# Optimization experiments

Measured on AMD Instinct MI355X. Metric: run time of the kernel, lower is better.

Reference implementation:

```python
import jax, jax.numpy as jnp
import numpy as np

NV, NA, T, FD, C, E = 192, 64, 128, 1024, 128, 262144
SPK = 3
N = (NV + NA) * T  # 32768 total graph nodes
NEG = -1e30


def _seg_max(msg, dst, mask):
    # masked scatter-max; PyG fills segments with no messages with 0
    m = jnp.where(mask[:, None], msg, NEG)
    out = jax.ops.segment_max(m, dst, num_segments=N)
    return jnp.where(out > NEG * 0.5, out, 0.0)


def _edge_conv(x, src, dst, mask, W1, b1, W2, b2):
    # EdgeConv: max_j MLP(cat[x_i, x_j - x_i])
    xi = x[dst]
    h = jnp.concatenate([xi, x[src] - xi], axis=-1)  # [E, 2C]
    h = jax.nn.relu(h @ W1 + b1) @ W2 + b2
    return _seg_max(h, dst, mask)


def _sage_conv(x, src, dst, mask, Wl, bl, Wr):
    # SAGEConv: lin_l(mean_j x_j) + lin_r(x_i), lin_r has no bias
    mf = mask.astype(x.dtype)
    s = jax.ops.segment_sum(x[src] * mf[:, None], dst, num_segments=N)
    cnt = jax.ops.segment_sum(mf, dst, num_segments=N)
    mean = s / jnp.maximum(cnt, 1.0)[:, None]
    return mean @ Wl + bl + x @ Wr


def setup_inputs():
    ks = jax.random.split(jax.random.key(0), 24)
    s = 0.05
    vals = jnp.array([-3, -2, -1, 0, 1, 3], jnp.int32)
    return {
        "x_visual": jax.random.normal(ks[0], (NV, T, FD), jnp.float32),
        "x_audio": jax.random.normal(ks[1], (NA, T, FD), jnp.float32),
        "W011": jax.random.normal(ks[2], (FD, C)) * s, "b011": jnp.zeros((C,)),
        "W012": jax.random.normal(ks[3], (FD, C)) * s, "b012": jnp.zeros((C,)),
        "ecA_W1": jax.random.normal(ks[4], (2 * C, C)) * s, "ecA_b1": jnp.zeros((C,)),
        "ecA_W2": jax.random.normal(ks[5], (C, C)) * s, "ecA_b2": jnp.zeros((C,)),
        "ec1_W1": jax.random.normal(ks[6], (2 * C, C)) * s, "ec1_b1": jnp.zeros((C,)),
        "ec1_W2": jax.random.normal(ks[7], (C, C)) * s, "ec1_b2": jnp.zeros((C,)),
        "ec2_W1": jax.random.normal(ks[8], (2 * C, C)) * s, "ec2_b1": jnp.zeros((C,)),
        "ec2_W2": jax.random.normal(ks[9], (C, C)) * s, "ec2_b2": jnp.zeros((C,)),
        "ec3_W1": jax.random.normal(ks[10], (2 * C, C)) * s, "ec3_b1": jnp.zeros((C,)),
        "ec3_W2": jax.random.normal(ks[11], (C, C)) * s, "ec3_b2": jnp.zeros((C,)),
        "sage_Wl": jax.random.normal(ks[12], (C, C)) * s, "sage_bl": jnp.zeros((C,)),
        "sage_Wr": jax.random.normal(ks[13], (C, C)) * s,
        "fc_W": jax.random.normal(ks[14], (C, 1)) * s, "fc_b": jnp.zeros((1,)),
        "edge_index": jax.random.randint(ks[15], (2, E), 0, N, dtype=jnp.int32),
        "edge_attr": vals[jax.random.randint(ks[16], (E,), 0, 6)],
        "speakers": SPK,
    }


def reference(x_visual, x_audio, W011, b011, W012, b012,
              ecA_W1, ecA_b1, ecA_W2, ecA_b2,
              ec1_W1, ec1_b1, ec1_W2, ec1_b2,
              ec2_W1, ec2_b1, ec2_W2, ec2_b2,
              ec3_W1, ec3_b1, ec3_W2, ec3_b2,
              sage_Wl, sage_bl, sage_Wr, fc_W, fc_b,
              edge_index, edge_attr, speakers):
    xv = x_visual @ W011 + b011          # [NV, T, C]
    xa = x_audio @ W012 + b012           # [NA, T, C]
    x = jnp.concatenate([xv, xa], axis=0).reshape(-1, C)  # [N, C]
    src, dst = edge_index[0], edge_index[1]
    m_audio = edge_attr == -2
    m_vpa = edge_attr == -3
    m_acv = edge_attr == 3
    m1 = (edge_attr >= 0) & (edge_attr <= 1)
    m2 = (edge_attr <= 0) & (edge_attr >= -1)
    m3 = jnp.abs(edge_attr) <= 1
    # Visual_Add_Audio_GNN: max-aggregate (x_i + x_j)
    xa_g = jax.nn.relu(_seg_max(x[dst] + x[src], dst, m_vpa))
    a = jax.nn.relu(_edge_conv(xa_g, src, dst, m_audio, ecA_W1, ecA_b1, ecA_W2, ecA_b2))
    a_res = a @ fc_W + fc_b              # [N, 1] per-node audio scores
    # Audio_Weight_Add_Visual_GNN: sum-aggregate (w_j * x_j + x_i)
    wmsg = jnp.where(m_acv[:, None], a_res[src] * x[src] + x[dst], 0.0)
    xv2 = jax.nn.relu(jax.ops.segment_sum(wmsg, dst, num_segments=N))

    def branch(mask, W1, b1, W2, b2):
        h = jax.nn.relu(_edge_conv(xv2, src, dst, mask, W1, b1, W2, b2))
        return jax.nn.relu(_sage_conv(h, src, dst, mask, sage_Wl, sage_bl, sage_Wr))

    xo = (branch(m1, ec1_W1, ec1_b1, ec1_W2, ec1_b2)
          + branch(m2, ec2_W1, ec2_b1, ec2_W2, ec2_b2)
          + branch(m3, ec3_W1, ec3_b1, ec3_W2, ec3_b2))
    # gather main-speaker visual nodes
    idx = (jnp.arange(0, NV * T, speakers * T)[:, None] + jnp.arange(T)).reshape(-1)
    return xo[idx]
```

## Files before the change

### kernel.cpp

```cpp
#include <hip/hip_runtime.h>
#include <cstdint>
#include <cstddef>

#define NVv 192
#define NAa 64
#define TT 128
#define FDd 1024
#define CCc 128
#define EEe 262144
#define NNn 32768

typedef _Float16 f16x8 __attribute__((ext_vector_type(8)));
typedef float f32x4 __attribute__((ext_vector_type(4)));

#define CAP0 65536
#define CAP1 65536
#define CAP2 65536
#define CAP3 98304
#define CAP4 98304
#define CAP5 147456
#define ARENA_TOTAL (CAP0+CAP1+CAP2+CAP3+CAP4+CAP5)
#define OFF0 0
#define OFF1 CAP0
#define OFF2 (CAP0+CAP1)
#define OFF3 (CAP0+CAP1+CAP2)
#define OFF4 (CAP0+CAP1+CAP2+CAP3)
#define OFF5 (CAP0+CAP1+CAP2+CAP3+CAP4)

__device__ __forceinline__ void eval_masks(int a, bool m[6]) {
    m[0] = (a == -3); m[1] = (a == -2); m[2] = (a == 3);
    m[3] = (a >= 0) & (a <= 1);
    m[4] = (a >= -1) & (a <= 0);
    m[5] = (a >= -1) & (a <= 1);
}

struct WSmall { const float* p[14]; };
struct PV3  { const _Float16* Wd[3]; const _Float16* Wv[3]; const float* b1[3];
              _Float16* P[3]; _Float16* V[3]; };
struct MLP3 { const _Float16* W2[3]; const float* b2[3];
              const _Float16* P[3]; const _Float16* V[3]; float* AH[3]; };

__global__ __launch_bounds__(256) void k_setup(
    const float* __restrict__ W011, const float* __restrict__ W012,
    WSmall wsm, _Float16* __restrict__ WT, _Float16* __restrict__ WTs,
    float* __restrict__ hf)
{
    int blk = blockIdx.x, tid = threadIdx.x;
    if (blk < 1024) {
        int idx = blk * 256 + tid;
        int which = idx >> 17;
        int r = idx & 131071;
        int n = r >> 10, k = r & 1023;
        const float* src = which ? W012 : W011;
        WT[idx] = (_Float16)src[k * 128 + n];
    } else if (blk < 1920) {
        int idx = (blk - 1024) * 256 + tid;
        int seg = idx >> 14;
        int r = idx & 16383;
        int n = r >> 7, k = r & 127;
        const float* src = wsm.p[seg];
        float v = src[k * 128 + n];
        if (seg < 12 && (seg % 3) == 0) v -= src[16384 + k * 128 + n];
        WTs[idx] = (_Float16)v;
    } else {
        size_t i = (size_t)(blk - 1920) * 1024 + (size_t)tid * 4;
        *(float4*)(hf + i) = make_float4(0.f, 0.f, 0.f, 0.f);
    }
}

__global__ __launch_bounds__(256) void k_hist(
    const int* __restrict__ attr, const int* __restrict__ edst,
    int* __restrict__ hist)
{
    int e = blockIdx.x * 256 + threadIdx.x;
    int a = attr[e], d = edst[e];
    bool m[6]; eval_masks(a, m);
#pragma unroll
    for (int j = 0; j < 6; ++j)
        if (m[j]) atomicAdd(&hist[j * NNn + d], 1);
}

__global__ __launch_bounds__(256) void k_scan_a(
    const int* __restrict__ hist, int* __restrict__ base, int* __restrict__ bsum)
{
    __shared__ int wsum[4];
    int idx = blockIdx.x * 256 + threadIdx.x;
    int tid = threadIdx.x, lane = tid & 63, wv = tid >> 6;
    int v = hist[idx];
    int x = v;
#pragma unroll
    for (int off = 1; off < 64; off <<= 1) {
        int y = __shfl_up(x, off, 64);
        if (lane >= off) x += y;
    }
    if (lane == 63) wsum[wv] = x;
    __syncthreads();
    int add = 0;
    for (int w = 0; w < wv; ++w) add += wsum[w];
    base[idx] = add + x - v;
    if (tid == 255) bsum[blockIdx.x] = add + x;
}

__global__ __launch_bounds__(384) void k_scan_b(int* __restrict__ bsum, int* __restrict__ cnts)
{
    int wv = threadIdx.x >> 6;
    int lane = threadIdx.x & 63;
    int run = 0;
#pragma unroll
    for (int c0 = 0; c0 < 128; c0 += 64) {
        int v = bsum[wv * 128 + c0 + lane];
        int x = v;
#pragma unroll
        for (int off = 1; off < 64; off <<= 1) {
            int y = __shfl_up(x, off, 64);
            if (lane >= off) x += y;
        }
        bsum[wv * 128 + c0 + lane] = run + (x - v);
        run += __shfl(x, 63, 64);
    }
    if (lane == 0) cnts[wv] = run;
}

__global__ __launch_bounds__(256) void k_scan_c(int* __restrict__ base, const int* __restrict__ bsum)
{
    base[blockIdx.x * 256 + threadIdx.x] += bsum[blockIdx.x];
}

__global__ __launch_bounds__(256) void k_fill_zero(
    const int* __restrict__ esrc, const int* __restrict__ edst,
    const int* __restrict__ attr, const int* __restrict__ base,
    int* __restrict__ fill, int2* __restrict__ arena, const int* __restrict__ hist,
    float* __restrict__ AH0, float* __restrict__ AH1,
    float* __restrict__ AH2, float* __restrict__ AH3)
{
    int blk = blockIdx.x, tid = threadIdx.x;
    if (blk < 1024) {
        int e = blk * 256 + tid;
        int a = attr[e];
        int s = esrc[e], d = edst[e];
        bool m[6]; eval_masks(a, m);
        const int caps[6] = {CAP0, CAP1, CAP2, CAP3, CAP4, CAP5};
        const int offs[6] = {OFF0, OFF1, OFF2, OFF3, OFF4, OFF5};
#pragma unroll
        for (int j = 0; j < 6; ++j) {
            if (m[j]) {
                int pos = base[j * NNn + d] + atomicAdd(&fill[j * NNn + d], 1);
                if (pos < caps[j]) arena[offs[j] + pos] = make_int2(s, d);
            }
        }
    } else {
        int zb = blk - 1024;
        int col = tid & 127, sub = tid >> 7;
        const int js[4] = {1, 3, 4, 5};
        float* AHs[4] = {AH0, AH1, AH2, AH3};
        for (int d = zb * 2 + sub; d < NNn; d += 2048 * 2) {
#pragma unroll
            for (int jj = 0; jj < 4; ++jj) {
                int j = js[jj];
                int c = hist[j * NNn + d];
                bool need;
                if (c == 0) need = true;
                else {
                    int b = base[j * NNn + d], e = b + c;
                    need = ((b & 63) == 0) || ((e & 63) == 0) || ((b >> 6) != ((e - 1) >> 6));
                }
                if (need) AHs[jj][(size_t)d * 128 + col] = 0.f;
            }
        }
    }
}

__global__ __launch_bounds__(512) void k_proj(
    const float* __restrict__ xv, const float* __restrict__ xa,
    const _Float16* __restrict__ BTv, const _Float16* __restrict__ BTa,
    float* __restrict__ Pp0, float* __restrict__ Pp1)
{
    __shared__ _Float16 Bl[2][128][136];
    const int tid = threadIdx.x, wave = tid >> 6, lane = tid & 63;
    const int tile = blockIdx.x >> 1, kh = blockIdx.x & 1;
    const float* A; const _Float16* BT; int mbase, obase;
    if (tile < 192) { A = xv; BT = BTv; mbase = tile * 128; obase = mbase; }
    else { A = xa; BT = BTa; mbase = (tile - 192) * 128; obase = 24576 + mbase; }
    float* Pout = kh ? Pp1 : Pp0;
    const int kbase = kh * 512;

    const int mrow = mbase + wave * 16 + (lane & 15);
    const int fk   = (lane >> 4) * 8;
    f32x4 acc[8];
#pragma unroll
    for (int i = 0; i < 8; ++i) acc[i] = (f32x4){0,0,0,0};

#pragma unroll
    for (int it = 0; it < 4; ++it) {
        int c = it * 512 + tid;
        int n = c >> 4, koff = (c & 15) * 8;
        *(f16x8*)&Bl[0][n][koff] = *(const f16x8*)(BT + (size_t)n * 1024 + kbase + koff);
    }
    f16x8 af[4];
#pragma unroll
    for (int t4 = 0; t4 < 4; ++t4) {
        const float* asrc = A + (size_t)mrow * 1024 + kbase + t4 * 32 + fk;
        float4 a0 = *(const float4*)asrc;
        float4 a1 = *(const float4*)(asrc + 4);
        af[t4] = (f16x8){ (_Float16)a0.x, (_Float16)a0.y, (_Float16)a0.z, (_Float16)a0.w,
                          (_Float16)a1.x, (_Float16)a1.y, (_Float16)a1.z, (_Float16)a1.w };
    }
    __syncthreads();

    for (int kc = 0; kc < 4; ++kc) {
        const int cur = kc & 1;
        f16x8 nf[4];
        if (kc < 3) {
            const int nxt = cur ^ 1;
#pragma unroll
            for (int it = 0; it < 4; ++it) {
                int c = it * 512 + tid;
                int n = c >> 4, koff = (c & 15) * 8;
                *(f16x8*)&Bl[nxt][n][koff] =
                    *(const f16x8*)(BT + (size_t)n * 1024 + kbase + (kc + 1) * 128 + koff);
            }
#pragma unroll
            for (int t4 = 0; t4 < 4; ++t4) {
                const float* asrc = A + (size_t)mrow * 1024 + kbase + (kc + 1) * 128 + t4 * 32 + fk;
                float4 a0 = *(const float4*)asrc;
                float4 a1 = *(const float4*)(asrc + 4);
                nf[t4] = (f16x8){ (_Float16)a0.x, (_Float16)a0.y, (_Float16)a0.z, (_Float16)a0.w,
                                  (_Float16)a1.x, (_Float16)a1.y, (_Float16)a1.z, (_Float16)a1.w };
            }
        }
#pragma unroll
        for (int t4 = 0; t4 < 4; ++t4)
#pragma unroll
            for (int nt = 0; nt < 8; ++nt) {
                f16x8 bf = *(const f16x8*)&Bl[cur][nt * 16 + (lane & 15)][t4 * 32 + fk];
                acc[nt] = __builtin_amdgcn_mfma_f32_16x16x32_f16(af[t4], bf, acc[nt], 0, 0, 0);
            }
        if (kc < 3) {
#pragma unroll
            for (int t4 = 0; t4 < 4; ++t4) af[t4] = nf[t4];
        }
        __syncthreads();
    }
    const int cbase = lane & 15, rloc = (lane >> 4) * 4;
    const int wgrp = wave & 3;
    float* Hsf = (float*)&Bl[0][0][0] + (size_t)wgrp * 16 * 132;
#pragma unroll
    for (int grp = 0; grp < 2; ++grp) {
        if ((wave >> 2) == grp) {
#pragma unroll
            for (int nt = 0; nt < 8; ++nt) {
                int c2 = nt * 16 + cbase;
#pragma unroll
                for (int rr = 0; rr < 4; ++rr)
                    Hsf[(rloc + rr) * 132 + c2] = acc[nt][rr];
            }
#pragma unroll
            for (int it = 0; it < 8; ++it) {
                int id = it * 64 + lane;
                int row = id >> 5, off = (id & 31) * 4;
                float4 v = *(float4*)&Hsf[row * 132 + off];
                *(float4*)&Pout[(size_t)(obase + wave * 16 + row) * 128 + off] = v;
            }
        }
        __syncthreads();
    }
}

__global__ __launch_bounds__(256) void k_reduce(
    const float* __restrict__ Pp0, const float* __restrict__ Pp1,
    const float* __restrict__ b011, const float* __restrict__ b012,
    float* __restrict__ X)
{
    size_t f = (size_t)blockIdx.x * 256 + threadIdx.x;
    size_t i = f * 4;
    int col = (int)(i & 127);
    int row = (int)(i >> 7);
    const float* bias = (row < 24576) ? b011 : b012;
    float4 a = *(const float4*)(Pp0 + i);
    float4 b = *(const float4*)(Pp1 + i);
    float4 bb = *(const float4*)(bias + col);
    *(float4*)(X + i) = make_float4(a.x + b.x + bb.x, a.y + b.y + bb.y,
                                    a.z + b.z + bb.z, a.w + b.w + bb.w);
}

__device__ __forceinline__ void pv_body(
    const float* __restrict__ A, const _Float16* __restrict__ BT1,
    const float* __restrict__ b1, const _Float16* __restrict__ BT2,
    _Float16* __restrict__ P, _Float16* __restrict__ V, int tileblk,
    _Float16 (*Bl1)[136], _Float16 (*Bl2)[136], float* bb)
{
    const int tid = threadIdx.x, wave = tid >> 6, lane = tid & 63;
    const int r0 = tileblk * 64 + wave * 16;
    const int fk = (lane >> 4) * 8;
    const int mrow = r0 + (lane & 15);
    float4 a0[4], a1[4];
#pragma unroll
    for (int t4 = 0; t4 < 4; ++t4) {
        const float* asrc = A + (size_t)mrow * 128 + t4 * 32 + fk;
        a0[t4] = *(const float4*)asrc;
        a1[t4] = *(const float4*)(asrc + 4);
    }
#pragma unroll
    for (int it = 0; it < 8; ++it) {
        int c = it * 256 + tid;
        int n = c >> 4, koff = (c & 15) * 8;
        *(f16x8*)&Bl1[n][koff] = *(const f16x8*)(BT1 + (size_t)n * 128 + koff);
        *(f16x8*)&Bl2[n][koff] = *(const f16x8*)(BT2 + (size_t)n * 128 + koff);
    }
    if (tid < 128) bb[tid] = b1[tid];
    __syncthreads();

    f16x8 af[4];
#pragma unroll
    for (int t4 = 0; t4 < 4; ++t4)
        af[t4] = (f16x8){ (_Float16)a0[t4].x, (_Float16)a0[t4].y, (_Float16)a0[t4].z, (_Float16)a0[t4].w,
                          (_Float16)a1[t4].x, (_Float16)a1[t4].y, (_Float16)a1[t4].z, (_Float16)a1[t4].w };
    f32x4 acc1[8], acc2[8];
#pragma unroll
    for (int i = 0; i < 8; ++i) { acc1[i] = (f32x4){0,0,0,0}; acc2[i] = (f32x4){0,0,0,0}; }
#pragma unroll
    for (int t4 = 0; t4 < 4; ++t4)
#pragma unroll
        for (int nt = 0; nt < 8; ++nt) {
            f16x8 bf1 = *(const f16x8*)&Bl1[nt * 16 + (lane & 15)][t4 * 32 + fk];
            f16x8 bf2 = *(const f16x8*)&Bl2[nt * 16 + (lane & 15)][t4 * 32 + fk];
            acc1[nt] = __builtin_amdgcn_mfma_f32_16x16x32_f16(af[t4], bf1, acc1[nt], 0, 0, 0);
            acc2[nt] = __builtin_amdgcn_mfma_f32_16x16x32_f16(af[t4], bf2, acc2[nt], 0, 0, 0);
        }
    __syncthreads();
    _Float16* Hs = &Bl1[0][0] + (size_t)wave * 16 * 136;
    const int cbase = lane & 15, rloc = (lane >> 4) * 4;
#pragma unroll
    for (int nt = 0; nt < 8; ++nt) {
        int c2 = nt * 16 + cbase;
        float bvv = bb[c2];
#pragma unroll
        for (int rr = 0; rr < 4; ++rr)
            Hs[(rloc + rr) * 136 + c2] = (_Float16)(acc1[nt][rr] + bvv);
    }
#pragma unroll
    for (int it = 0; it < 4; ++it) {
        int id = it * 64 + lane;
        int row = id >> 4, koff = (id & 15) * 8;
        *(f16x8*)&P[(size_t)(r0 + row) * 128 + koff] = *(f16x8*)&Hs[row * 136 + koff];
    }
#pragma unroll
    for (int nt = 0; nt < 8; ++nt) {
        int c2 = nt * 16 + cbase;
#pragma unroll
        for (int rr = 0; rr < 4; ++rr)
            Hs[(rloc + rr) * 136 + c2] = (_Float16)acc2[nt][rr];
    }
#pragma unroll
    for (int it = 0; it < 4; ++it) {
        int id = it * 64 + lane;
        int row = id >> 4, koff = (id & 15) * 8;
        *(f16x8*)&V[(size_t)(r0 + row) * 128 + koff] = *(f16x8*)&Hs[row * 136 + koff];
    }
}

__global__ __launch_bounds__(256) void k_pv(
    const float* __restrict__ A, const _Float16* __restrict__ BT1,
    const float* __restrict__ b1, const _Float16* __restrict__ BT2,
    _Float16* __restrict__ P, _Float16* __restrict__ V)
{
    __shared__ _Float16 Bl1[128][136];
    __shared__ _Float16 Bl2[128][136];
    __shared__ float bb[128];
    pv_body(A, BT1, b1, BT2, P, V, blockIdx.x, Bl1, Bl2, bb);
}

__global__ __launch_bounds__(256) void k_pv3(const float* __restrict__ A, PV3 p)
{
    __shared__ _Float16 Bl1[128][136];
    __shared__ _Float16 Bl2[128][136];
    __shared__ float bb[128];
    int b = blockIdx.x >> 9, t = blockIdx.x & 511;
    pv_body(A, p.Wd[b], p.b1[b], p.Wv[b], p.P[b], p.V[b], t, Bl1, Bl2, bb);
}

__device__ __forceinline__ void mlp_tile(
    const _Float16* __restrict__ P, const _Float16* __restrict__ V,
    const _Float16* __restrict__ W2T, const float* __restrict__ b2,
    const int2* __restrict__ list, int cnt, int t, float* __restrict__ agg,
    _Float16 (*Rl)[136], _Float16 (*W2l)[136], float* b2l,
    int2* eSD, unsigned char* gstart, int* gdst, int* ngrS)
{
    const int tid  = threadIdx.x;
    const int wave = tid >> 6;
    const int lane = tid & 63;
#pragma unroll
    for (int i = 0; i < 8; ++i) {
        int c = tid + i * 256;
        int n = c >> 4, koff = (c & 15) * 8;
        *(f16x8*)&W2l[n][koff] = *(const f16x8*)(W2T + n * 128 + koff);
    }
    if (tid < 128) b2l[tid] = b2[tid];
    if (tid < 64) {
        int e = t * 64 + tid;
        eSD[tid] = (e < cnt) ? list[e] : make_int2(0, -1);
    }
    __syncthreads();
    if (tid < 64) {
        int d = eSD[tid].y;
        bool flag = (tid == 0) || (d != eSD[tid - 1].y);
        unsigned long long bm = __ballot(flag);
        int rank = (int)__popcll(bm & ((1ull << tid) - 1ull));
        if (flag) { gstart[rank] = (unsigned char)tid; gdst[rank] = d; }
        if (tid == 0) {
            int ng = (int)__popcll(bm);
            *ngrS = ng;
            gstart[ng] = 64;
        }
    }
    const int rrow = tid >> 4;
    const int rch  = (tid & 15) * 8;
#pragma unroll
    for (int p = 0; p < 4; ++p) {
        int i = p * 16 + rrow;
        int2 sd = eSD[i];
        f16x8 rv = {0, 0, 0, 0, 0, 0, 0, 0};
        if (sd.y >= 0) {
            f16x8 pv = *(const f16x8*)(P + (size_t)sd.y * 128 + rch);
            f16x8 vv = *(const f16x8*)(V + (size_t)sd.x * 128 + rch);
            rv = pv + vv;
#pragma unroll
            for (int q = 0; q < 8; ++q)
                rv[q] = (rv[q] > (_Float16)0.f) ? rv[q] : (_Float16)0.f;
        }
        *(f16x8*)&Rl[i][rch] = rv;
    }
    __syncthreads();

    const int frow  = wave * 16 + (lane & 15);
    const int fq    = (lane >> 4) * 8;
    f32x4 acc[8];
#pragma unroll
    for (int i = 0; i < 8; ++i) acc[i] = (f32x4){0,0,0,0};
#pragma unroll
    for (int t4 = 0; t4 < 4; ++t4) {
        f16x8 af = *(const f16x8*)&Rl[frow][t4 * 32 + fq];
#pragma unroll
        for (int nt = 0; nt < 8; ++nt) {
            f16x8 bf = *(const f16x8*)&W2l[nt * 16 + (lane & 15)][t4 * 32 + fq];
            acc[nt] = __builtin_amdgcn_mfma_f32_16x16x32_f16(af, bf, acc[nt], 0, 0, 0);
        }
    }
    __syncthreads();
    const int rbase = wave * 16 + (lane >> 4) * 4;
    const int cbase = lane & 15;
#pragma unroll
    for (int nt = 0; nt < 8; ++nt) {
        int c2 = nt * 16 + cbase;
        float bv = b2l[c2];
#pragma unroll
        for (int rr = 0; rr < 4; ++rr)
            Rl[rbase + rr][c2] = (_Float16)fmaxf(acc[nt][rr] + bv, 0.f);
    }
    __syncthreads();
    const int col  = tid & 127;
    const int half = tid >> 7;
    int ng = *ngrS;
    for (int g = half; g < ng; g += 2) {
        int s = gstart[g], e = gstart[g + 1];
        int d = gdst[g];
        if (d < 0) continue;
        float m = 0.f;
        for (int i = s; i < e; ++i)
            m = fmaxf(m, (float)Rl[i][col]);
        size_t o = (size_t)d * 128 + col;
        if (s == 0 || e == 64)
            atomicMax((unsigned int*)&agg[o], __float_as_uint(m));
        else
            agg[o] = m;
    }
}

__global__ __launch_bounds__(256, 3) void k_edge_mlp(
    const _Float16* __restrict__ P, const _Float16* __restrict__ V,
    const _Float16* __restrict__ W2T, const float* __restrict__ b2,
    const int2* __restrict__ list, const int* __restrict__ cntp, int cap,
    float* __restrict__ agg)
{
    __shared__ _Float16 Rl[64][136];
    __shared__ _Float16 W2l[128][136];
    __shared__ float b2l[128];
    __shared__ int2 eSD[64];
    __shared__ unsigned char gstart[66];
    __shared__ int gdst[64];
    __shared__ int ngrS;
    int cnt = min(*cntp, cap);
    int ntiles = (cnt + 63) >> 6;
    if ((int)blockIdx.x >= ntiles) return;
    for (int t = blockIdx.x; t < ntiles; t += gridDim.x) {
        if (t != (int)blockIdx.x) __syncthreads();
        mlp_tile(P, V, W2T, b2, list, cnt, t, agg,
                 Rl, W2l, b2l, eSD, gstart, gdst, &ngrS);
    }
}

__global__ __launch_bounds__(256, 3) void k_edge_mlp3(
    MLP3 p, const int2* __restrict__ arena, const int* __restrict__ cnts)
{
    __shared__ _Float16 Rl[64][136];
    __shared__ _Float16 W2l[128][136];
    __shared__ float b2l[128];
    __shared__ int2 eSD[64];
    __shared__ unsigned char gstart[66];
    __shared__ int gdst[64];
    __shared__ int ngrS;
    const int caps[3] = {CAP3, CAP4, CAP5};
    const int offs[3] = {OFF3, OFF4, OFF5};
    int c0 = min(cnts[3], CAP3), c1 = min(cnts[4], CAP4), c2 = min(cnts[5], CAP5);
    int n0 = (c0 + 63) >> 6, n1 = (c1 + 63) >> 6, n2 = (c2 + 63) >> 6;
    int t = blockIdx.x, b;
    if (t < n0) b = 0;
    else if (t < n0 + n1) { b = 1; t -= n0; }
    else if (t < n0 + n1 + n2) { b = 2; t -= n0 + n1; }
    else return;
    int cnt = min(cnts[3 + b], caps[b]);
    mlp_tile(p.P[b], p.V[b], p.W2[b], p.b2[b], arena + offs[b], cnt, t, p.AH[b],
             Rl, W2l, b2l, eSD, gstart, gdst, &ngrS);
}

__global__ __launch_bounds__(256) void k_csr_vpa(
    const float* __restrict__ X, const int2* __restrict__ list,
    const int* __restrict__ base, const int* __restrict__ cntarr, int cap,
    float* __restrict__ S)
{
    int col = threadIdx.x & 127;
    int sub = threadIdx.x >> 7;
    for (int d = blockIdx.x * 2 + sub; d < NNn; d += gridDim.x * 2) {
        int c = cntarr[d];
        float v = 0.f;
        if (c > 0) {
            int b = base[d];
            int end = min(b + c, cap);
            float mx = -3.0e38f;
            for (int i = b; i < end; ++i)
                mx = fmaxf(mx, X[(size_t)list[i].x * 128 + col]);
            v = fmaxf(X[(size_t)d * 128 + col] + mx, 0.f);
        }
        S[(size_t)d * 128 + col] = v;
    }
}

__global__ __launch_bounds__(256) void k_csr_acv(
    const float* __restrict__ X, const float* __restrict__ ares,
    const int2* __restrict__ list,
    const int* __restrict__ base, const int* __restrict__ cntarr, int cap,
    float* __restrict__ S)
{
    int col = threadIdx.x & 127;
    int sub = threadIdx.x >> 7;
    for (int d = blockIdx.x * 2 + sub; d < NNn; d += gridDim.x * 2) {
        int c = cntarr[d];
        float v = 0.f;
        if (c > 0) {
            int b = base[d];
            int end = min(b + c, cap);
            float s = 0.f;
            for (int i = b; i < end; ++i) {
                int sr = list[i].x;
                s += ares[sr] * X[(size_t)sr * 128 + col];
            }
            v = fmaxf(s + (float)c * X[(size_t)d * 128 + col], 0.f);
        }
        S[(size_t)d * 128 + col] = v;
    }
}

__global__ __launch_bounds__(256) void k_meanc3(
    float* const AH1, float* const AH2, float* const AH3,
    const int2* __restrict__ arena,
    const int* __restrict__ base, const int* __restrict__ hist,
    const int* __restrict__ spk, int ntarg,
    float* __restrict__ S1c, float* __restrict__ AHc)
{
    int col = threadIdx.x & 127;
    int sub = threadIdx.x >> 7;
    int step = spk[0] * TT;
    const int caps[3] = {CAP3, CAP4, CAP5};
    const int offs[3] = {OFF3, OFF4, OFF5};
    const float* AHs[3] = {AH1, AH2, AH3};
    int total = 3 * ntarg;
    for (int ci2 = blockIdx.x * 2 + sub; ci2 < total; ci2 += gridDim.x * 2) {
        int b = ci2 / ntarg;
        int ci = ci2 - b * ntarg;
        int j = 3 + b;
        const float* AH = AHs[b];
        const int2* list = arena + offs[b];
        int d = (ci >> 7) * step + (ci & 127);
        int c = hist[j * NNn + d];
        float v = 0.f;
        if (c > 0) {
            int bs = base[j * NNn + d];
            int end = min(bs + c, caps[b]);
            float s = 0.f;
            for (int i = bs; i < end; ++i)
                s += AH[(size_t)list[i].x * 128 + col];
            v = s / (float)c;
        }
        S1c[(size_t)ci2 * 128 + col] = v;
        AHc[(size_t)ci2 * 128 + col] = AH[(size_t)d * 128 + col];
    }
}

__global__ __launch_bounds__(256) void k_fc(
    const float* __restrict__ A, const float* __restrict__ W,
    const float* __restrict__ b, float* __restrict__ ares)
{
    int node = blockIdx.x * 4 + (threadIdx.x >> 6);
    int lane = threadIdx.x & 63;
    const float* row = A + (size_t)node * 128;
    float v = row[lane] * W[lane] + row[lane + 64] * W[lane + 64];
#pragma unroll
    for (int off = 32; off > 0; off >>= 1) v += __shfl_down(v, off, 64);
    if (lane == 0) ares[node] = v + b[0];
}

__global__ __launch_bounds__(256) void k_sage_out(
    const float* __restrict__ S1c, const float* __restrict__ AHc,
    const _Float16* __restrict__ WlT, const _Float16* __restrict__ WrT,
    const float* __restrict__ bl, float* __restrict__ out, int ntarg)
{
    __shared__ _Float16 Al[64][40];
    __shared__ _Float16 Bl[128][40];
    const int tid  = threadIdx.x;
    const int wave = tid >> 6;
    const int lane = tid & 63;
    const int m0   = blockIdx.x * 64;

    f32x4 accB[8], accO[8];
#pragma unroll
    for (int i = 0; i < 8; ++i) { accB[i] = (f32x4){0,0,0,0}; accO[i] = (f32x4){0,0,0,0}; }

    const int ar = tid >> 2;
    const int ak = (tid & 3) * 8;
    const int fr = wave * 16 + (lane & 15);
    const int fk = (lane >> 4) * 8;
    const int rbase = wave * 16 + (lane >> 4) * 4;
    const int cbase = lane & 15;

    for (int seg = 0; seg < 6; ++seg) {
        int b = seg >> 1, which = seg & 1;
        const float* A = (which ? AHc : S1c) + (size_t)b * ntarg * 128;
        const _Float16* BT = which ? WrT : WlT;
        for (int k0 = 0; k0 < 128; k0 += 32) {
            __syncthreads();
            const float* asrc = A + (size_t)(m0 + ar) * 128 + (k0 + ak);
            float4 a0 = *(const float4*)asrc;
            float4 a1 = *(const float4*)(asrc + 4);
            f16x8 av = { (_Float16)a0.x, (_Float16)a0.y, (_Float16)a0.z, (_Float16)a0.w,
                         (_Float16)a1.x, (_Float16)a1.y, (_Float16)a1.z, (_Float16)a1.w };
            *(f16x8*)&Al[ar][ak] = av;
#pragma unroll
            for (int i = 0; i < 2; ++i) {
                int c = tid + i * 256;
                int n = c >> 2, koff = (c & 3) * 8;
                *(f16x8*)&Bl[n][koff] = *(const f16x8*)(BT + (size_t)n * 128 + k0 + koff);
            }
            __syncthreads();
            f16x8 af = *(const f16x8*)&Al[fr][fk];
#pragma unroll
            for (int nt = 0; nt < 8; ++nt) {
                f16x8 bf = *(const f16x8*)&Bl[nt * 16 + (lane & 15)][fk];
                accB[nt] = __builtin_amdgcn_mfma_f32_16x16x32_f16(af, bf, accB[nt], 0, 0, 0);
            }
        }
        if (which) {
#pragma unroll
            for (int nt = 0; nt < 8; ++nt) {
                int col = nt * 16 + cbase;
                float bv = bl[col];
#pragma unroll
                for (int rr = 0; rr < 4; ++rr) {
                    accO[nt][rr] += fmaxf(accB[nt][rr] + bv, 0.f);
                    accB[nt][rr] = 0.f;
                }
            }
        }
    }
#pragma unroll
    for (int nt = 0; nt < 8; ++nt) {
        int col = nt * 16 + cbase;
#pragma unroll
        for (int rr = 0; rr < 4; ++rr)
            out[(size_t)(m0 + rbase + rr) * 128 + col] = accO[nt][rr];
    }
}

extern "C" void kernel_launch(void* const* d_in, const int* in_sizes, int n_in,
                              void* d_out, int out_size, void* d_ws, size_t ws_size,
                              hipStream_t stream)
{
    (void)in_sizes; (void)n_in; (void)ws_size;
    const float* xv   = (const float*)d_in[0];
    const float* xa   = (const float*)d_in[1];
    const float* W011 = (const float*)d_in[2];
    const float* b011 = (const float*)d_in[3];
    const float* W012 = (const float*)d_in[4];
    const float* b012 = (const float*)d_in[5];
    const float* ecW1[4] = {(const float*)d_in[6],  (const float*)d_in[10],
                            (const float*)d_in[14], (const float*)d_in[18]};
    const float* ecb1[4] = {(const float*)d_in[7],  (const float*)d_in[11],
                            (const float*)d_in[15], (const float*)d_in[19]};
    const float* ecW2[4] = {(const float*)d_in[8],  (const float*)d_in[12],
                            (const float*)d_in[16], (const float*)d_in[20]};
    const float* ecb2[4] = {(const float*)d_in[9],  (const float*)d_in[13],
                            (const float*)d_in[17], (const float*)d_in[21]};
    const float* sageWl = (const float*)d_in[22];
    const float* sagebl = (const float*)d_in[23];
    const float* sageWr = (const float*)d_in[24];
    const float* fcW    = (const float*)d_in[25];
    const float* fcb    = (const float*)d_in[26];
    const int*   esrc   = (const int*)d_in[27];
    const int*   edst   = esrc + EEe;
    const int*   attr   = (const int*)d_in[28];
    const int*   spk    = (const int*)d_in[29];
    float* out = (float*)d_out;
    const int ntarg = out_size >> 7;

    const size_t NC = (size_t)NNn * CCc;
    float* ws   = (float*)d_ws;
    float* X    = ws;
    float* S1   = ws + 1 * NC;
    float* XV2  = ws + 2 * NC;
    float* AHc  = ws + 3 * NC;
    float* AH0  = ws + 4 * NC;
    float* AH1  = ws + 5 * NC;
    float* AH2  = ws + 6 * NC;
    float* AH3  = ws + 7 * NC;
    _Float16* P0 = (_Float16*)(ws + 8 * NC);
    _Float16* V0 = P0 + NC;
    _Float16* P1 = (_Float16*)X;
    _Float16* V1 = P1 + NC;
    _Float16* P2 = (_Float16*)AHc;
    _Float16* V2 = P2 + NC;
    float* ARES = ws + 9 * NC;
    int*   cnts = (int*)(ARES + NNn);
    int*   bsum = cnts + 16;
    int*   hist = bsum + 1024;
    int*   fill = hist + 6 * NNn;
    int*   base = fill + 6 * NNn;
    int2*  arena = (int2*)(base + 6 * NNn);
    _Float16* WT = (_Float16*)(arena + ARENA_TOTAL);

    const _Float16* W011T = WT;
    const _Float16* W012T = WT + 131072;
    _Float16* WTs = WT + 262144;
    const _Float16* WlT   = WTs + 12 * 16384;
    const _Float16* WrT   = WTs + 13 * 16384;

    WSmall wsm;
    for (int i = 0; i < 4; ++i) {
        wsm.p[3*i + 0] = ecW1[i];
        wsm.p[3*i + 1] = ecW1[i] + 16384;
        wsm.p[3*i + 2] = ecW2[i];
    }
    wsm.p[12] = sageWl; wsm.p[13] = sageWr;
    k_setup<<<2304, 256, 0, stream>>>(W011, W012, wsm, WT, WTs, (float*)hist);
    k_hist<<<EEe / 256, 256, 0, stream>>>(attr, edst, hist);
    k_scan_a<<<768, 256, 0, stream>>>(hist, base, bsum);
    k_scan_b<<<1, 384, 0, stream>>>(bsum, cnts);
    k_scan_c<<<768, 256, 0, stream>>>(base, bsum);
    k_fill_zero<<<3072, 256, 0, stream>>>(esrc, edst, attr, base, fill, arena, hist,
                                          AH0, AH1, AH2, AH3);

    k_proj<<<512, 512, 0, stream>>>(xv, xa, W011T, W012T, S1, XV2);
    k_reduce<<<(int)(NC / 1024), 256, 0, stream>>>(S1, XV2, b011, b012, X);
    k_csr_vpa<<<2048, 256, 0, stream>>>(X, arena + OFF0, base + 0 * NNn,
                                        hist + 0 * NNn, CAP0, S1);
    k_pv<<<512, 256, 0, stream>>>(S1, WTs, ecb1[0], WTs + 16384, P0, V0);
    k_edge_mlp<<<2048, 256, 0, stream>>>(P0, V0, WTs + 2 * 16384, ecb2[0],
                                         arena + OFF1, cnts + 1, CAP1, AH0);
    k_fc<<<NNn / 4, 256, 0, stream>>>(AH0, fcW, fcb, ARES);
    k_csr_acv<<<2048, 256, 0, stream>>>(X, ARES, arena + OFF2, base + 2 * NNn,
                                        hist + 2 * NNn, CAP2, XV2);
    PV3 pv3;
    MLP3 m3;
    _Float16* Pb[3] = {P0, P1, P2};
    _Float16* Vb[3] = {V0, V1, V2};
    float* AHb[3] = {AH1, AH2, AH3};
    for (int b = 0; b < 3; ++b) {
        _Float16* Wd = WTs + (3 * (b + 1)) * 16384;
        pv3.Wd[b] = Wd; pv3.Wv[b] = Wd + 16384; pv3.b1[b] = ecb1[b + 1];
        pv3.P[b] = Pb[b]; pv3.V[b] = Vb[b];
        m3.W2[b] = Wd + 2 * 16384; m3.b2[b] = ecb2[b + 1];
        m3.P[b] = Pb[b]; m3.V[b] = Vb[b]; m3.AH[b] = AHb[b];
    }
    k_pv3<<<1536, 256, 0, stream>>>(XV2, pv3);
    k_edge_mlp3<<<5376, 256, 0, stream>>>(m3, arena, cnts);
    k_meanc3<<<2048, 256, 0, stream>>>(AH1, AH2, AH3, arena, base, hist,
                                       spk, ntarg, S1, AHc);
    k_sage_out<<<ntarg / 64, 256, 0, stream>>>(S1, AHc, WlT, WrT, sagebl, out, ntarg);
}
```

Baseline: 520.3 us.

## Make edge-MLP kernels persistent with two-team blocks sharing one W2 load

The edge-MLP kernels become persistent 512-thread blocks: two 256-thread teams each process their own 64-edge tile while sharing a single W2 tile loaded into LDS once per block, instead of reloading weights for every tile. The fused three-branch kernel uses a fixed per-branch grid split (146/146/220 blocks) and loops over tiles with a grid stride. The LDS row pad changes from 136 to 132 halves. This cuts repeated weight staging and block launch overhead, but risks load imbalance from the fixed grid split, reduced occupancy, and possible LDS bank conflicts from the new padding. Within a team, the tile loop's reuse of shared buffers across iterations relies on barriers inside the tile routine that are not visible here.

```diff
diff --git a/kernel.cpp b/kernel.cpp
--- a/kernel.cpp
+++ b/kernel.cpp
@@ -26,6 +26,8 @@
 #define OFF3 (CAP0+CAP1+CAP2)
 #define OFF4 (CAP0+CAP1+CAP2+CAP3)
 #define OFF5 (CAP0+CAP1+CAP2+CAP3+CAP4)
+
+#define MPAD 132
 
 __device__ __forceinline__ void eval_masks(int a, bool m[6]) {
     m[0] = (a == -3); m[1] = (a == -2); m[2] = (a == 3);
@@ -379,23 +381,30 @@
     pv_body(A, p.Wd[b], p.b1[b], p.Wv[b], p.P[b], p.V[b], t, Bl1, Bl2, bb);
 }
 
-__device__ __forceinline__ void mlp_tile(
-    const _Float16* __restrict__ P, const _Float16* __restrict__ V,
+__device__ __forceinline__ void mlp_loadW(
     const _Float16* __restrict__ W2T, const float* __restrict__ b2,
-    const int2* __restrict__ list, int cnt, int t, float* __restrict__ agg,
-    _Float16 (*Rl)[136], _Float16 (*W2l)[136], float* b2l,
-    int2* eSD, unsigned char* gstart, int* gdst, int* ngrS)
-{
-    const int tid  = threadIdx.x;
-    const int wave = tid >> 6;
-    const int lane = tid & 63;
-#pragma unroll
-    for (int i = 0; i < 8; ++i) {
-        int c = tid + i * 256;
+    _Float16 (*W2l)[MPAD], float* __restrict__ b2l)
+{
+    int tid = threadIdx.x;
+#pragma unroll
+    for (int i = 0; i < 4; ++i) {
+        int c = tid + i * 512;
         int n = c >> 4, koff = (c & 15) * 8;
         *(f16x8*)&W2l[n][koff] = *(const f16x8*)(W2T + n * 128 + koff);
     }
     if (tid < 128) b2l[tid] = b2[tid];
+}
+
+__device__ __forceinline__ void mlp_tile2(
+    const _Float16* __restrict__ P, const _Float16* __restrict__ V,
+    const int2* __restrict__ list, int cnt, int t, float* __restrict__ agg,
+    _Float16 (*Rl)[MPAD], const _Float16 (*W2l)[MPAD], const float* __restrict__ b2l,
+    int2* __restrict__ eSD, unsigned char* __restrict__ gstart,
+    int* __restrict__ gdst, int* __restrict__ ngrS)
+{
+    const int tid  = threadIdx.x & 255;
+    const int wave = tid >> 6;
+    const int lane = threadIdx.x & 63;
     if (tid < 64) {
         int e = t * 64 + tid;
         eSD[tid] = (e < cnt) ? list[e] : make_int2(0, -1);
@@ -476,51 +485,62 @@
     }
 }
 
-__global__ __launch_bounds__(256, 3) void k_edge_mlp(
+__global__ __launch_bounds__(512, 2) void k_edge_mlp(
     const _Float16* __restrict__ P, const _Float16* __restrict__ V,
     const _Float16* __restrict__ W2T, const float* __restrict__ b2,
     const int2* __restrict__ list, const int* __restrict__ cntp, int cap,
     float* __restrict__ agg)
 {
-    __shared__ _Float16 Rl[64][136];
-    __shared__ _Float16 W2l[128][136];
+    __shared__ _Float16 W2l[128][MPAD];
     __shared__ float b2l[128];
-    __shared__ int2 eSD[64];
-    __shared__ unsigned char gstart[66];
-    __shared__ int gdst[64];
-    __shared__ int ngrS;
+    __shared__ _Float16 Rl[2][64][MPAD];
+    __shared__ int2 eSD[2][64];
+    __shared__ unsigned char gstart[2][68];
+    __shared__ int gdst[2][64];
+    __shared__ int ngrS[2];
     int cnt = min(*cntp, cap);
     int ntiles = (cnt + 63) >> 6;
-    if ((int)blockIdx.x >= ntiles) return;
-    for (int t = blockIdx.x; t < ntiles; t += gridDim.x) {
-        if (t != (int)blockIdx.x) __syncthreads();
-        mlp_tile(P, V, W2T, b2, list, cnt, t, agg,
-                 Rl, W2l, b2l, eSD, gstart, gdst, &ngrS);
-    }
-}
-
-__global__ __launch_bounds__(256, 3) void k_edge_mlp3(
+    if ((int)blockIdx.x * 2 >= ntiles) return;
+    mlp_loadW(W2T, b2, W2l, b2l);
+    const int team = threadIdx.x >> 8;
+    for (int base = blockIdx.x * 2; base < ntiles; base += gridDim.x * 2) {
+        mlp_tile2(P, V, list, cnt, base + team, agg,
+                  Rl[team], W2l, b2l, eSD[team], gstart[team], gdst[team], &ngrS[team]);
+    }
+}
+
+#define MLP3_G0 146
+#define MLP3_G1 146
+#define MLP3_G2 220
+#define MLP3_GRID (MLP3_G0 + MLP3_G1 + MLP3_G2)
+
+__global__ __launch_bounds__(512, 2) void k_edge_mlp3(
     MLP3 p, const int2* __restrict__ arena, const int* __restrict__ cnts)
 {
-    __shared__ _Float16 Rl[64][136];
-    __shared__ _Float16 W2l[128][136];
+    __shared__ _Float16 W2l[128][MPAD];
     __shared__ float b2l[128];
-    __shared__ int2 eSD[64];
-    __shared__ unsigned char gstart[66];
-    __shared__ int gdst[64];
-    __shared__ int ngrS;
+    __shared__ _Float16 Rl[2][64][MPAD];
+    __shared__ int2 eSD[2][64];
+    __shared__ unsigned char gstart[2][68];
+    __shared__ int gdst[2][64];
+    __shared__ int ngrS[2];
     const int caps[3] = {CAP3, CAP4, CAP5};
     const int offs[3] = {OFF3, OFF4, OFF5};
-    int c0 = min(cnts[3], CAP3), c1 = min(cnts[4], CAP4), c2 = min(cnts[5], CAP5);
-    int n0 = (c0 + 63) >> 6, n1 = (c1 + 63) >> 6, n2 = (c2 + 63) >> 6;
-    int t = blockIdx.x, b;
-    if (t < n0) b = 0;
-    else if (t < n0 + n1) { b = 1; t -= n0; }
-    else if (t < n0 + n1 + n2) { b = 2; t -= n0 + n1; }
-    else return;
+    int blk = blockIdx.x;
+    int b, i, G;
+    if (blk < MLP3_G0)                 { b = 0; i = blk;                       G = MLP3_G0; }
+    else if (blk < MLP3_G0 + MLP3_G1)  { b = 1; i = blk - MLP3_G0;             G = MLP3_G1; }
+    else                               { b = 2; i = blk - (MLP3_G0 + MLP3_G1); G = MLP3_G2; }
     int cnt = min(cnts[3 + b], caps[b]);
-    mlp_tile(p.P[b], p.V[b], p.W2[b], p.b2[b], arena + offs[b], cnt, t, p.AH[b],
-             Rl, W2l, b2l, eSD, gstart, gdst, &ngrS);
+    int ntiles = (cnt + 63) >> 6;
+    if (i * 2 >= ntiles) return;
+    mlp_loadW(p.W2[b], p.b2[b], W2l, b2l);
+    const int team = threadIdx.x >> 8;
+    const int2* list = arena + offs[b];
+    for (int base = i * 2; base < ntiles; base += G * 2) {
+        mlp_tile2(p.P[b], p.V[b], list, cnt, base + team, p.AH[b],
+                  Rl[team], W2l, b2l, eSD[team], gstart[team], gdst[team], &ngrS[team]);
+    }
 }
 
 __global__ __launch_bounds__(256) void k_csr_vpa(
@@ -772,8 +792,8 @@
     k_csr_vpa<<<2048, 256, 0, stream>>>(X, arena + OFF0, base + 0 * NNn,
                                         hist + 0 * NNn, CAP0, S1);
     k_pv<<<512, 256, 0, stream>>>(S1, WTs, ecb1[0], WTs + 16384, P0, V0);
-    k_edge_mlp<<<2048, 256, 0, stream>>>(P0, V0, WTs + 2 * 16384, ecb2[0],
-                                         arena + OFF1, cnts + 1, CAP1, AH0);
+    k_edge_mlp<<<512, 512, 0, stream>>>(P0, V0, WTs + 2 * 16384, ecb2[0],
+                                        arena + OFF1, cnts + 1, CAP1, AH0);
     k_fc<<<NNn / 4, 256, 0, stream>>>(AH0, fcW, fcb, ARES);
     k_csr_acv<<<2048, 256, 0, stream>>>(X, ARES, arena + OFF2, base + 2 * NNn,
                                         hist + 2 * NNn, CAP2, XV2);
@@ -790,7 +810,7 @@
         m3.P[b] = Pb[b]; m3.V[b] = Vb[b]; m3.AH[b] = AHb[b];
     }
     k_pv3<<<1536, 256, 0, stream>>>(XV2, pv3);
-    k_edge_mlp3<<<5376, 256, 0, stream>>>(m3, arena, cnts);
+    k_edge_mlp3<<<MLP3_GRID, 512, 0, stream>>>(m3, arena, cnts);
     k_meanc3<<<2048, 256, 0, stream>>>(AH1, AH2, AH3, arena, base, hist,
                                        spk, ntarg, S1, AHc);
     k_sage_out<<<ntarg / 64, 256, 0, stream>>>(S1, AHc, WlT, WrT, sagebl, out, ntarg);
```

Result: slower. 596.1 us (+14.6%).
